# Kernel optimization log

Measured on AMD Instinct MI355X. Metric: run time of the kernel, lower is better.

Reference implementation:

```python
import jax, jax.numpy as jnp
import numpy as np

KERNEL_MUL = 2.0
KERNEL_NUM = 5


def _mmd(src, tar):
    """Multi-bandwidth Gaussian-kernel MMD, matching torch MMDLoss.mmd."""
    B = src.shape[0]
    total = jnp.concatenate([src, tar], axis=0)          # [2B, D]
    sq = jnp.sum(total * total, axis=1)                  # [2B]
    # ||a-b||^2 = ||a||^2 + ||b||^2 - 2 a.b  (GEMM form of the broadcast subtract)
    dist = sq[:, None] + sq[None, :] - 2.0 * (total @ total.T)  # [2B, 2B]
    n = 2 * B
    # torch uses L2_distance.data -> bandwidth is detached from the graph
    bandwidth = jax.lax.stop_gradient(jnp.sum(dist)) / (n * n - n)
    bandwidth = bandwidth / (KERNEL_MUL ** (KERNEL_NUM // 2))
    kernel = sum(jnp.exp(-dist / (bandwidth * KERNEL_MUL ** k)) for k in range(KERNEL_NUM))
    XX = kernel[:B, :B]
    YY = kernel[B:, B:]
    XY = kernel[:B, B:]
    YX = kernel[B:, :B]
    return jnp.mean(XX + YY - XY - YX)


def setup_inputs() -> dict:
    key = jax.random.key(0)
    k1, k2, k3 = jax.random.split(key, 3)
    B, IN, OUT, L = 4096, 512, 256, 2
    x = jax.random.normal(k1, (B, IN), dtype=jnp.float32)
    W_aux = jax.random.normal(k2, (L, IN), dtype=jnp.float32) * (1.0 / np.sqrt(IN))
    b_aux = jnp.zeros((L,), dtype=jnp.float32)
    W = jax.random.normal(k3, (L, OUT, IN), dtype=jnp.float32) * (1.0 / np.sqrt(IN))
    b = jnp.zeros((L, OUT), dtype=jnp.float32)
    return {"x": x, "W_aux": W_aux, "b_aux": b_aux, "W": W, "b": b}


def reference(x, W_aux, b_aux, W, b):
    L = W.shape[0]
    gates = jax.nn.softmax(x @ W_aux.T + b_aux, axis=-1)      # [B, L]
    outs = jnp.einsum('bi,loi->blo', x, W) + b                # [B, L, out]
    combine = jnp.einsum('bl,blo->bo', gates, outs)           # soft-gated combine
    loss = 0.0
    for i in range(L):
        for j in range(i + 1, L):
            loss = loss + _mmd(outs[:, i, :], outs[:, j, :])
    inter_mmd = loss * 2.0 / (L * L - L)
    return combine, -inter_mmd
```

## Files before the change

### kernel.cpp

```cpp
#include <hip/hip_runtime.h>
#include <stdint.h>
#include <math.h>

typedef __attribute__((ext_vector_type(8))) __bf16 bf16x8;
typedef __attribute__((ext_vector_type(4))) __bf16 bf16x4;
typedef __attribute__((ext_vector_type(4))) float f32x4;

__device__ __forceinline__ void gload_lds16(const __bf16* g, __bf16* l) {
  __builtin_amdgcn_global_load_lds(
      (const __attribute__((address_space(1))) unsigned int*)g,
      (__attribute__((address_space(3))) unsigned int*)l,
      16, 0, 0);
}

__global__ __launch_bounds__(256) void k_gates(const float* __restrict__ x,
                                               const float* __restrict__ Waux,
                                               const float* __restrict__ baux,
                                               float* __restrict__ gates,
                                               float* __restrict__ colsum,
                                               float* __restrict__ scal) {
  if (blockIdx.x == 0) {
    colsum[threadIdx.x] = 0.f;
    if (threadIdx.x < 8) scal[threadIdx.x] = 0.f;
  }
  const int wave = threadIdx.x >> 6;
  const int lane = threadIdx.x & 63;
  const int row = blockIdx.x * 4 + wave;
  const float4* xr = (const float4*)(x + (size_t)row * 512);
  const float4* w0 = (const float4*)(Waux);
  const float4* w1 = (const float4*)(Waux + 512);
  float p0 = 0.f, p1 = 0.f;
  for (int c = lane; c < 128; c += 64) {
    float4 xv = xr[c];
    float4 a = w0[c], b = w1[c];
    p0 += xv.x * a.x + xv.y * a.y + xv.z * a.z + xv.w * a.w;
    p1 += xv.x * b.x + xv.y * b.y + xv.z * b.z + xv.w * b.w;
  }
  for (int off = 32; off; off >>= 1) {
    p0 += __shfl_down(p0, off, 64);
    p1 += __shfl_down(p1, off, 64);
  }
  if (lane == 0) {
    p0 += baux[0]; p1 += baux[1];
    float m = fmaxf(p0, p1);
    float e0 = __expf(p0 - m), e1 = __expf(p1 - m);
    float inv = 1.f / (e0 + e1);
    gates[row * 2 + 0] = e0 * inv;
    gates[row * 2 + 1] = e1 * inv;
  }
}

__global__ __launch_bounds__(256) void k_outs(const float* __restrict__ x,
                                              const float* __restrict__ W,
                                              const float* __restrict__ bias,
                                              __bf16* __restrict__ totalbf) {
  __shared__ __bf16 As[64][64];
  __shared__ __bf16 Bs[64][64];
  const int bj = blockIdx.x;
  const int bi = blockIdx.y;
  const int t = threadIdx.x;
  const int wid = t >> 6, lane = t & 63;
  const int wr = wid >> 1, wc = wid & 1;
  const int n16 = lane & 15, q = lane >> 4;
  const int sx = (n16 & 7) << 3;
  const int erow = t >> 4;
  const int c4 = (t & 15) << 2;

  f32x4 acc[2][2];
  f32x4 zero = {0.f, 0.f, 0.f, 0.f};
  for (int i = 0; i < 2; ++i)
    for (int j = 0; j < 2; ++j) acc[i][j] = zero;

  const int arow0 = bi * 64, brow0 = bj * 64;

  float4 ra[4], rb[4];
#pragma unroll
  for (int p = 0; p < 4; ++p) {
    int row = p * 16 + erow;
    ra[p] = *(const float4*)(x + (size_t)(arow0 + row) * 512 + c4);
    rb[p] = *(const float4*)(W + (size_t)(brow0 + row) * 512 + c4);
  }

  for (int kc = 0; kc < 512; kc += 64) {
#pragma unroll
    for (int p = 0; p < 4; ++p) {
      int row = p * 16 + erow;
      int col = c4 ^ ((row & 7) << 3);
      float4 va = ra[p];
      bf16x4 ba = {(__bf16)va.x, (__bf16)va.y, (__bf16)va.z, (__bf16)va.w};
      *(bf16x4*)&As[row][col] = ba;
      float4 vb = rb[p];
      bf16x4 bb = {(__bf16)vb.x, (__bf16)vb.y, (__bf16)vb.z, (__bf16)vb.w};
      *(bf16x4*)&Bs[row][col] = bb;
    }
    __syncthreads();
    if (kc < 448) {
#pragma unroll
      for (int p = 0; p < 4; ++p) {
        int row = p * 16 + erow;
        ra[p] = *(const float4*)(x + (size_t)(arow0 + row) * 512 + kc + 64 + c4);
        rb[p] = *(const float4*)(W + (size_t)(brow0 + row) * 512 + kc + 64 + c4);
      }
    }
#pragma unroll
    for (int ks = 0; ks < 2; ++ks) {
      bf16x8 af[2], bfr[2];
#pragma unroll
      for (int f = 0; f < 2; ++f) {
        af[f]  = *(const bf16x8*)&As[wr * 32 + f * 16 + n16][(ks * 32 + q * 8) ^ sx];
        bfr[f] = *(const bf16x8*)&Bs[wc * 32 + f * 16 + n16][(ks * 32 + q * 8) ^ sx];
      }
      for (int fr = 0; fr < 2; ++fr)
        for (int fc = 0; fc < 2; ++fc)
          acc[fr][fc] = __builtin_amdgcn_mfma_f32_16x16x32_bf16(af[fr], bfr[fc], acc[fr][fc], 0, 0, 0);
    }
    __syncthreads();
  }

  for (int fc = 0; fc < 2; ++fc) {
    int n_g = bj * 64 + wc * 32 + fc * 16 + n16;
    float bv = bias[n_g];
    int l = n_g >> 8, o = n_g & 255;
    for (int fr = 0; fr < 2; ++fr) {
      for (int r = 0; r < 4; ++r) {
        int m_g = bi * 64 + wr * 32 + fr * 16 + q * 4 + r;
        float v = acc[fr][fc][r] + bv;
        totalbf[(size_t)(l * 4096 + m_g) * 256 + o] = (__bf16)v;
      }
    }
  }
}

__global__ __launch_bounds__(256) void k_sqc(const __bf16* __restrict__ tot,
                                             const float* __restrict__ gates,
                                             float* __restrict__ sq,
                                             float* __restrict__ colsum,
                                             float* __restrict__ scal,
                                             float* __restrict__ out) {
  __shared__ float lcol[4][256];
  __shared__ float wsq[4];
  __shared__ unsigned int isLast;
  const int t = threadIdx.x;
  const int wave = t >> 6, lane = t & 63;
  float c0 = 0.f, c1 = 0.f, c2 = 0.f, c3 = 0.f;
  float bsq = 0.f;
  for (int it = 0; it < 8; ++it) {
    int m = blockIdx.x * 32 + wave * 8 + it;
    bf16x4 v0 = *(const bf16x4*)(tot + (size_t)m * 256 + lane * 4);
    bf16x4 v1 = *(const bf16x4*)(tot + (size_t)(4096 + m) * 256 + lane * 4);
    float f00 = v0[0], f01 = v0[1], f02 = v0[2], f03 = v0[3];
    float f10 = v1[0], f11 = v1[1], f12 = v1[2], f13 = v1[3];
    float s0 = f00 * f00 + f01 * f01 + f02 * f02 + f03 * f03;
    float s1 = f10 * f10 + f11 * f11 + f12 * f12 + f13 * f13;
    for (int off = 32; off; off >>= 1) {
      s0 += __shfl_down(s0, off, 64);
      s1 += __shfl_down(s1, off, 64);
    }
    if (lane == 0) { sq[m] = s0; sq[4096 + m] = s1; bsq += s0 + s1; }
    c0 += f00 + f10; c1 += f01 + f11; c2 += f02 + f12; c3 += f03 + f13;
    float2 gv = *(const float2*)(gates + m * 2);
    float4 r;
    r.x = gv.x * f00 + gv.y * f10;
    r.y = gv.x * f01 + gv.y * f11;
    r.z = gv.x * f02 + gv.y * f12;
    r.w = gv.x * f03 + gv.y * f13;
    *(float4*)(out + (size_t)m * 256 + lane * 4) = r;
  }
  lcol[wave][lane * 4 + 0] = c0;
  lcol[wave][lane * 4 + 1] = c1;
  lcol[wave][lane * 4 + 2] = c2;
  lcol[wave][lane * 4 + 3] = c3;
  if (lane == 0) wsq[wave] = bsq;
  __syncthreads();
  float s2 = lcol[0][t] + lcol[1][t] + lcol[2][t] + lcol[3][t];
  atomicAdd(&colsum[t], s2);
  if (t == 0) atomicAdd(&scal[4], wsq[0] + wsq[1] + wsq[2] + wsq[3]);
  __threadfence();
  if (t == 0) {
    unsigned int c = atomicAdd((unsigned int*)(scal + 5), 1u);
    isLast = (c == 127u) ? 1u : 0u;
  }
  __syncthreads();
  if (isLast) {
    __threadfence();
    float cv = atomicAdd(&colsum[t], 0.0f);
    lcol[0][t] = cv * cv;
    __syncthreads();
    for (int off = 128; off; off >>= 1) {
      if (t < off) lcol[0][t] += lcol[0][t + off];
      __syncthreads();
    }
    if (t == 0) {
      float sumsq = atomicAdd(&scal[4], 0.0f);
      double sumdist = 2.0 * 8192.0 * (double)sumsq - 2.0 * (double)lcol[0][0];
      double bw = sumdist / (8192.0 * 8192.0 - 8192.0) / 4.0;
      scal[1] = (float)(1.4426950408889634 / (bw * 16.0));
      scal[2] = (float)bw;
    }
  }
}

__global__ __launch_bounds__(256) void k_gram(const __bf16* __restrict__ tot,
                                              const float* __restrict__ sq,
                                              const float* __restrict__ scal,
                                              float* __restrict__ Ssum,
                                              float* __restrict__ out) {
  const int b = blockIdx.x;
  const int nid = (b & 7) * 260 + (b >> 3);
  int ti = (int)((129.0 - sqrt(129.0 * 129.0 - 8.0 * (double)nid)) * 0.5);
  while (64 * ti - ti * (ti - 1) / 2 > nid) --ti;
  while (64 * (ti + 1) - (ti + 1) * ti / 2 <= nid) ++ti;
  const int tj = ti + (nid - (64 * ti - ti * (ti - 1) / 2));

  __shared__ __bf16 As[2][128][64];
  __shared__ __bf16 Bs[2][128][64];
  __shared__ float sqi[128], sqj[128];
  __shared__ float wred[4];
  const int t = threadIdx.x;
  const int wid = t >> 6, lane = t & 63;
  const int wr = wid >> 1, wc = wid & 1;
  const int n16 = lane & 15, q = lane >> 4;
  const int sx = (n16 & 7) << 3;
  const int lr = lane >> 3;
  const int ls = lane & 7;

  const float g = scal[1];
  if (t < 128) sqi[t] = sq[ti * 128 + t] * g;
  else         sqj[t - 128] = sq[tj * 128 + (t - 128)] * g;

  f32x4 acc[4][4];
  f32x4 zero = {0.f, 0.f, 0.f, 0.f};
  for (int i = 0; i < 4; ++i)
    for (int j = 0; j < 4; ++j) acc[i][j] = zero;

  const __bf16* gA = tot + (size_t)(ti * 128 + wid * 32 + lr) * 256 + ((ls ^ lr) << 3);
  const __bf16* gB = tot + (size_t)(tj * 128 + wid * 32 + lr) * 256 + ((ls ^ lr) << 3);

#pragma unroll
  for (int p = 0; p < 4; ++p) {
    gload_lds16(gA + p * 8 * 256, &As[0][wid * 32 + p * 8][0]);
    gload_lds16(gB + p * 8 * 256, &Bs[0][wid * 32 + p * 8][0]);
  }

#pragma unroll
  for (int it = 0; it < 4; ++it) {
    const int cur = it & 1;
    if (it < 3) {
      const int kc = (it + 1) * 64;
#pragma unroll
      for (int p = 0; p < 4; ++p) {
        gload_lds16(gA + p * 8 * 256 + kc, &As[cur ^ 1][wid * 32 + p * 8][0]);
        gload_lds16(gB + p * 8 * 256 + kc, &Bs[cur ^ 1][wid * 32 + p * 8][0]);
      }
    }
    if (it < 3) asm volatile("s_waitcnt vmcnt(8)" ::: "memory");
    else        asm volatile("s_waitcnt vmcnt(0)" ::: "memory");
    __builtin_amdgcn_s_barrier();
    __builtin_amdgcn_sched_barrier(0);
    __builtin_amdgcn_s_setprio(1);
#pragma unroll
    for (int ks = 0; ks < 2; ++ks) {
      bf16x8 af[4], bfr[4];
#pragma unroll
      for (int f = 0; f < 4; ++f) {
        af[f]  = *(const bf16x8*)&As[cur][wr * 64 + f * 16 + n16][(ks * 32 + q * 8) ^ sx];
        bfr[f] = *(const bf16x8*)&Bs[cur][wc * 64 + f * 16 + n16][(ks * 32 + q * 8) ^ sx];
      }
      for (int fr = 0; fr < 4; ++fr)
        for (int fc = 0; fc < 4; ++fc)
          acc[fr][fc] = __builtin_amdgcn_mfma_f32_16x16x32_bf16(af[fr], bfr[fc], acc[fr][fc], 0, 0, 0);
    }
    __builtin_amdgcn_s_setprio(0);
    asm volatile("s_waitcnt lgkmcnt(0)" ::: "memory");
    __builtin_amdgcn_sched_barrier(0);
    __builtin_amdgcn_s_barrier();
  }

  const float twog = 2.f * g;
  float lsum = 0.f;
  for (int fr = 0; fr < 4; ++fr) {
    for (int r = 0; r < 4; ++r) {
      float gsi = sqi[wr * 64 + fr * 16 + q * 4 + r];
      for (int fc = 0; fc < 4; ++fc) {
        float gsj = sqj[wc * 64 + fc * 16 + n16];
        float u = exp2f(fmaf(twog, acc[fr][fc][r], -(gsi + gsj)));
        float u2 = u * u, u4 = u2 * u2, u8 = u4 * u4;
        float s1 = fmaf(u8, u8, u8);
        lsum += (u + u2) + (u4 + s1);
      }
    }
  }
  for (int off = 32; off; off >>= 1) lsum += __shfl_down(lsum, off, 64);
  if (lane == 0) wred[wid] = lsum;
  __syncthreads();
  if (t == 0) {
    float blocksum = wred[0] + wred[1] + wred[2] + wred[3];
    float sgn = ((ti < 32) == (tj < 32)) ? 1.f : -1.f;
    float wgt = (ti == tj) ? sgn : 2.f * sgn;
    atomicAdd(Ssum, wgt * blocksum);
    __threadfence();
    unsigned int* cnt = (unsigned int*)(Ssum + 3);
    unsigned int c = atomicAdd(cnt, 1u);
    if (c == 2079u) {
      float totS = atomicAdd(Ssum, 0.0f);
      out[1048576] = -(totS / 16777216.0f);
    }
  }
}

extern "C" void kernel_launch(void* const* d_in, const int* in_sizes, int n_in,
                              void* d_out, int out_size, void* d_ws, size_t ws_size,
                              hipStream_t stream) {
  const float* x    = (const float*)d_in[0];
  const float* Waux = (const float*)d_in[1];
  const float* baux = (const float*)d_in[2];
  const float* W    = (const float*)d_in[3];
  const float* bias = (const float*)d_in[4];
  float* out = (float*)d_out;

  char* ws = (char*)d_ws;
  __bf16* totalbf = (__bf16*)ws;
  float* sq      = (float*)(ws + 4194304);
  float* colsum  = (float*)(ws + 4227072);
  float* scal    = (float*)(ws + 4228096);
  float* gates   = (float*)(ws + 4228160);

  k_gates<<<1024, 256, 0, stream>>>(x, Waux, baux, gates, colsum, scal);
  k_outs<<<dim3(8, 64), 256, 0, stream>>>(x, W, bias, totalbf);
  k_sqc<<<128, 256, 0, stream>>>(totalbf, gates, sq, colsum, scal, out);
  k_gram<<<2080, 256, 0, stream>>>(totalbf, sq, scal, scal, out);
}
```

Before: 173.0 us.

## Load Gram MFMA fragments directly from global memory instead of LDS staging

```diff
diff --git a/kernel.cpp b/kernel.cpp
--- a/kernel.cpp
+++ b/kernel.cpp
@@ -5,13 +5,6 @@
 typedef __attribute__((ext_vector_type(8))) __bf16 bf16x8;
 typedef __attribute__((ext_vector_type(4))) __bf16 bf16x4;
 typedef __attribute__((ext_vector_type(4))) float f32x4;
-
-__device__ __forceinline__ void gload_lds16(const __bf16* g, __bf16* l) {
-  __builtin_amdgcn_global_load_lds(
-      (const __attribute__((address_space(1))) unsigned int*)g,
-      (__attribute__((address_space(3))) unsigned int*)l,
-      16, 0, 0);
-}
 
 __global__ __launch_bounds__(256) void k_gates(const float* __restrict__ x,
                                                const float* __restrict__ Waux,
@@ -212,17 +205,12 @@
   while (64 * (ti + 1) - (ti + 1) * ti / 2 <= nid) ++ti;
   const int tj = ti + (nid - (64 * ti - ti * (ti - 1) / 2));
 
-  __shared__ __bf16 As[2][128][64];
-  __shared__ __bf16 Bs[2][128][64];
   __shared__ float sqi[128], sqj[128];
   __shared__ float wred[4];
   const int t = threadIdx.x;
   const int wid = t >> 6, lane = t & 63;
   const int wr = wid >> 1, wc = wid & 1;
   const int n16 = lane & 15, q = lane >> 4;
-  const int sx = (n16 & 7) << 3;
-  const int lr = lane >> 3;
-  const int ls = lane & 7;
 
   const float g = scal[1];
   if (t < 128) sqi[t] = sq[ti * 128 + t] * g;
@@ -233,48 +221,23 @@
   for (int i = 0; i < 4; ++i)
     for (int j = 0; j < 4; ++j) acc[i][j] = zero;
 
-  const __bf16* gA = tot + (size_t)(ti * 128 + wid * 32 + lr) * 256 + ((ls ^ lr) << 3);
-  const __bf16* gB = tot + (size_t)(tj * 128 + wid * 32 + lr) * 256 + ((ls ^ lr) << 3);
-
-#pragma unroll
-  for (int p = 0; p < 4; ++p) {
-    gload_lds16(gA + p * 8 * 256, &As[0][wid * 32 + p * 8][0]);
-    gload_lds16(gB + p * 8 * 256, &Bs[0][wid * 32 + p * 8][0]);
-  }
-
-#pragma unroll
-  for (int it = 0; it < 4; ++it) {
-    const int cur = it & 1;
-    if (it < 3) {
-      const int kc = (it + 1) * 64;
-#pragma unroll
-      for (int p = 0; p < 4; ++p) {
-        gload_lds16(gA + p * 8 * 256 + kc, &As[cur ^ 1][wid * 32 + p * 8][0]);
-        gload_lds16(gB + p * 8 * 256 + kc, &Bs[cur ^ 1][wid * 32 + p * 8][0]);
-      }
-    }
-    if (it < 3) asm volatile("s_waitcnt vmcnt(8)" ::: "memory");
-    else        asm volatile("s_waitcnt vmcnt(0)" ::: "memory");
-    __builtin_amdgcn_s_barrier();
-    __builtin_amdgcn_sched_barrier(0);
-    __builtin_amdgcn_s_setprio(1);
-#pragma unroll
-    for (int ks = 0; ks < 2; ++ks) {
-      bf16x8 af[4], bfr[4];
-#pragma unroll
-      for (int f = 0; f < 4; ++f) {
-        af[f]  = *(const bf16x8*)&As[cur][wr * 64 + f * 16 + n16][(ks * 32 + q * 8) ^ sx];
-        bfr[f] = *(const bf16x8*)&Bs[cur][wc * 64 + f * 16 + n16][(ks * 32 + q * 8) ^ sx];
-      }
-      for (int fr = 0; fr < 4; ++fr)
-        for (int fc = 0; fc < 4; ++fc)
-          acc[fr][fc] = __builtin_amdgcn_mfma_f32_16x16x32_bf16(af[fr], bfr[fc], acc[fr][fc], 0, 0, 0);
-    }
-    __builtin_amdgcn_s_setprio(0);
-    asm volatile("s_waitcnt lgkmcnt(0)" ::: "memory");
-    __builtin_amdgcn_sched_barrier(0);
-    __builtin_amdgcn_s_barrier();
-  }
+  const __bf16* pA = tot + (size_t)(ti * 128 + wr * 64 + n16) * 256 + q * 8;
+  const __bf16* pB = tot + (size_t)(tj * 128 + wc * 64 + n16) * 256 + q * 8;
+
+#pragma unroll
+  for (int ks = 0; ks < 8; ++ks) {
+    bf16x8 af[4], bfr[4];
+#pragma unroll
+    for (int f = 0; f < 4; ++f) {
+      af[f]  = *(const bf16x8*)(pA + (size_t)f * 16 * 256 + ks * 32);
+      bfr[f] = *(const bf16x8*)(pB + (size_t)f * 16 * 256 + ks * 32);
+    }
+    for (int fr = 0; fr < 4; ++fr)
+      for (int fc = 0; fc < 4; ++fc)
+        acc[fr][fc] = __builtin_amdgcn_mfma_f32_16x16x32_bf16(af[fr], bfr[fc], acc[fr][fc], 0, 0, 0);
+  }
+
+  __syncthreads();
 
   const float twog = 2.f * g;
   float lsum = 0.f;
```

Measured after the change: 196.8 us. 13.7% more time.
